# Kernel tuning notes

Hardware: AMD Instinct MI355X
Metric: run time of the kernel (lower is better)

The kernel has to match this reference:

```python
import jax, jax.numpy as jnp
import numpy as np

B, N = 128, 256
EPS = float(np.finfo(np.float32).eps)  # torch clamp_probs epsilon for fp32


def to_z(logits, u):
    # torch.distributions.utils.clamp_probs + Gumbel perturbation
    uc = jnp.clip(u, EPS, 1.0 - EPS)
    return logits + (-jnp.log(-jnp.log(uc)))


def _find_cycle(heads):
    # heads[j] = parent of j; node 0 is the root (heads[0] == 0).
    L = len(heads)
    color = np.zeros(L, dtype=np.int8)  # 0 unvisited, 1 on path, 2 done
    color[0] = 2
    for start in range(1, L):
        if color[start]:
            continue
        path = []
        v = start
        while color[v] == 0:
            color[v] = 1
            path.append(v)
            v = int(heads[v])
        if color[v] == 1:  # found a cycle
            i = path.index(v)
            return path[i:]
        for p in path:
            color[p] = 2
    return None


def _chu_liu(score):
    # score[h, d] = weight of edge h -> d; diag and column 0 are -inf.
    L = score.shape[0]
    heads = score.argmax(axis=0)
    heads[0] = 0
    cyc = _find_cycle(heads)
    if cyc is None:
        return heads
    cyc = np.asarray(cyc)
    mask = np.ones(L, dtype=bool)
    mask[cyc] = False
    non = np.where(mask)[0]  # includes root 0
    n = len(non)
    cyc_head_sc = score[heads[cyc], cyc]  # [|C|] chosen in-edge weights of cycle nodes
    # contracted score matrix: nodes = non-cycle nodes + one supernode (index n)
    new = np.full((n + 1, n + 1), -np.inf, dtype=score.dtype)
    new[:n, :n] = score[np.ix_(non, non)]
    into = score[np.ix_(non, cyc)] - cyc_head_sc[None, :]  # gain of entering cycle at each node
    arg_into = into.argmax(axis=1)
    new[:n, n] = into[np.arange(n), arg_into]
    outo = score[np.ix_(cyc, non)]
    arg_out = outo.argmax(axis=0)
    new[n, :n] = outo[arg_out, np.arange(n)]
    nh = _chu_liu(new)
    # expand
    heads_out = np.empty(L, dtype=np.int64)
    nh_non = nh[:n]
    safe = np.clip(nh_non, 0, n - 1)
    heads_out[non] = np.where(nh_non == n, cyc[arg_out], non[safe])
    heads_out[cyc] = heads[cyc]
    hc = int(nh[n])  # head of the contracted supernode (index into non)
    heads_out[cyc[arg_into[hc]]] = non[hc]  # break the cycle at the entry node
    heads_out[0] = 0
    return heads_out


def edmonds_batch(z, lengths):
    # z: np [B, N, N] edge scores z[b, h, d]; root = node 0; per-graph size lengths[b].
    Bn, Nn, _ = z.shape
    arb = np.zeros((Bn, Nn, Nn), dtype=np.float32)
    stats = np.zeros((Bn,), dtype=np.float32)
    for b in range(Bn):  # irregular sequential graph algorithm: per-graph host loop
        L = int(lengths[b])
        s = z[b, :L, :L].astype(np.float64).copy()
        np.fill_diagonal(s, -np.inf)
        s[:, 0] = -np.inf  # no incoming edges to root
        heads = _chu_liu(s)
        deps = np.arange(1, L)
        arb[b, heads[deps], deps] = 1.0
        stats[b] = z[b, heads[deps], deps].sum()
    return jnp.asarray(arb), jnp.asarray(stats)


def setup_inputs():
    key = jax.random.key(0)
    k1, k2, k3 = jax.random.split(key, 3)
    logits = jax.random.normal(k1, (B, N, N), dtype=jnp.float32)
    u = jax.random.uniform(k2, (B, N, N), dtype=jnp.float32)
    lengths = jax.random.randint(k3, (B,), 2, N + 1, dtype=jnp.int32)
    return {"logits": logits, "u": u, "lengths": lengths}


def reference(logits, u, lengths):
    z = to_z(logits, u)  # Gumbel-perturbed scores (differentiable part)
    arb, stats = edmonds_batch(np.asarray(z), np.asarray(lengths))
    return (arb, stats, z)
```

## Files before the change

### kernel.cpp

```cpp
#include <hip/hip_runtime.h>
#include <cmath>

static constexpr int Bn = 128;
static constexpr int Nn = 256;
static constexpr int META_PB = 131072;

template <typename T>
__global__ __launch_bounds__(256) void zinit_kernel(
    const float* __restrict__ logits,
    const float* __restrict__ u,
    float* __restrict__ zout,
    float* __restrict__ arb,
    T* __restrict__ M)
{
    int idx = blockIdx.x * blockDim.x + threadIdx.x;
    int j = idx & (Nn - 1);
    int i = (idx >> 8) & (Nn - 1);
    const float EPS = 1.1920928955078125e-07f;
    float uv = u[idx];
    uv = fminf(fmaxf(uv, EPS), 1.0f - EPS);
    float z = logits[idx] - logf(-logf(uv));
    zout[idx] = z;
    arb[idx] = 0.0f;
    M[idx] = (i == j || j == 0) ? (T)(-INFINITY) : (T)z;
}

template <typename T>
__global__ __launch_bounds__(256) void edmonds_kernel(
    const int* __restrict__ lengths,
    const float* __restrict__ zout,
    T* __restrict__ Mg,
    unsigned char* __restrict__ metag,
    float* __restrict__ arb,
    float* __restrict__ stats)
{
    const int b = blockIdx.x;
    const int t = threadIdx.x;
    const int lane = t & 63, wv = t >> 6;
    T* M = Mg + (size_t)b * (Nn * Nn);
    unsigned char* meta = metag + (size_t)b * META_PB;
    const float* zb = zout + (size_t)b * (Nn * Nn);

    __shared__ unsigned short act[256];
    __shared__ unsigned short h[256];
    __shared__ unsigned short h2[256];
    __shared__ unsigned short p1[256];
    __shared__ unsigned short p2[256];
    __shared__ unsigned short inv_[256];
    __shared__ unsigned short cyc_c[256];
    __shared__ unsigned short non_c[256];
    __shared__ unsigned short cslot_s[256];
    __shared__ unsigned short resc[256];
    __shared__ unsigned short lev_n[256], lev_c[256];
    __shared__ int lev_off[256];
    __shared__ unsigned char in_cyc[256];
    __shared__ T hval[256];
    __shared__ T chs[256];
    __shared__ double red[256];
    __shared__ unsigned wmin[4];
    __shared__ int wcnt[4];
    __shared__ int sh_clen, sh_cnt, sh_wslot;

    const int L = lengths[b];

    act[t] = (unsigned short)t;
    if (t < L) {
        T best = -INFINITY; int bi = 0;
        const T* col = M + t;
        int i = 0;
        for (; i + 8 <= L; i += 8) {
            T v[8];
            #pragma unroll
            for (int k = 0; k < 8; ++k) v[k] = col[(i + k) * Nn];
            #pragma unroll
            for (int k = 0; k < 8; ++k)
                if (v[k] > best) { best = v[k]; bi = i + k; }
        }
        for (; i < L; ++i) {
            T v = col[i * Nn];
            if (v > best) { best = v; bi = i; }
        }
        h[t] = (t == 0) ? (unsigned short)0 : (unsigned short)bi;
        hval[t] = best;
    }
    __syncthreads();

    int Lc = L, depth = 0, moff = 0;

    while (true) {
        in_cyc[t] = 0;
        if (t < Lc) p1[t] = h[t];
        __syncthreads();

        const int rounds = 32 - __clz(Lc - 1);
        unsigned short* pa = p1;
        unsigned short* pb = p2;
        for (int r = 0; r < rounds; ++r) {
            if (t < Lc) pb[t] = pa[pa[t]];
            __syncthreads();
            unsigned short* tmp = pa; pa = pb; pb = tmp;
        }

        unsigned cand = (t >= 1 && t < Lc && pa[t] != 0) ? (unsigned)t : 0xFFFFu;
        for (int m = 1; m < 64; m <<= 1)
            cand = min(cand, (unsigned)__shfl_xor((int)cand, m));
        if (lane == 0) wmin[wv] = cand;
        __syncthreads();
        const unsigned vstar = min(min(wmin[0], wmin[1]), min(wmin[2], wmin[3]));
        if (vstar == 0xFFFFu) break;

        if (t == 0) {
            int w = pa[vstar];
            int cl = 0, v = w;
            do { cyc_c[cl++] = (unsigned short)v; in_cyc[v] = 1; v = h[v]; }
            while (v != w);
            sh_clen = cl;
            sh_wslot = act[w];
            sh_cnt = 0;
        }
        __syncthreads();
        const int clen = sh_clen;
        const int n = Lc - clen;
        const int wslot = sh_wslot;

        const bool fl = (t < Lc) && !in_cyc[t];
        unsigned long long mask = __ballot(fl);
        if (lane == 0) wcnt[wv] = __popcll(mask);
        __syncthreads();
        if (fl) {
            int base = 0;
            for (int k = 0; k < wv; ++k) base += wcnt[k];
            int pos = base + __popcll(mask & ((1ull << lane) - 1ull));
            non_c[pos] = (unsigned short)t;
            inv_[t] = (unsigned short)pos;
        }
        if (t < clen) {
            const int cc = cyc_c[t];
            chs[t] = hval[cc];
            cslot_s[t] = act[cc];
        }
        __syncthreads();

        T vin_r = (T)0, vout_r = (T)0;
        unsigned char argin_r = 0, argout_r = 0;
        int slot_r = 0;
        if (t < n) {
            slot_r = act[non_c[t]];
            T bv = -INFINITY; int bi = 0;
            T bo = -INFINITY; int bj = 0;
            int c = 0;
            for (; c + 4 <= clen; c += 4) {
                int cs[4]; T ch[4];
                #pragma unroll
                for (int k = 0; k < 4; ++k) { cs[k] = cslot_s[c + k]; ch[k] = chs[c + k]; }
                T vi[4], vo[4];
                #pragma unroll
                for (int k = 0; k < 4; ++k) {
                    vi[k] = M[slot_r * Nn + cs[k]] - ch[k];
                    vo[k] = M[cs[k] * Nn + slot_r];
                }
                #pragma unroll
                for (int k = 0; k < 4; ++k) {
                    if (vi[k] > bv) { bv = vi[k]; bi = c + k; }
                    if (vo[k] > bo) { bo = vo[k]; bj = c + k; }
                }
            }
            for (; c < clen; ++c) {
                const int cs = cslot_s[c];
                T vi = M[slot_r * Nn + cs] - chs[c];
                T vo = M[cs * Nn + slot_r];
                if (vi > bv) { bv = vi; bi = c; }
                if (vo > bo) { bo = vo; bj = c; }
            }
            vin_r = bv; argin_r = (unsigned char)bi;
            vout_r = bo; argout_r = (unsigned char)bj;
        }

        unsigned char* mp = meta + moff;
        if (t < n) {
            mp[t] = (unsigned char)non_c[t];
            mp[n + t] = argin_r;
            mp[2 * n + t] = argout_r;
            M[slot_r * Nn + wslot] = vin_r;
            M[wslot * Nn + slot_r] = vout_r;
        }
        if (t < clen) {
            mp[3 * n + t] = (unsigned char)cyc_c[t];
            mp[3 * n + clen + t] = (unsigned char)h[cyc_c[t]];
        }
        if (t == 0) {
            M[wslot * Nn + wslot] = (T)(-INFINITY);
            lev_n[depth] = (unsigned short)n;
            lev_c[depth] = (unsigned short)clen;
            lev_off[depth] = moff;
        }
        unsigned short myact = 0, myh = 0; T myhval = (T)0; bool need = false;
        if (t < n) {
            const int oc = non_c[t];
            myact = act[oc];
            const int ho = h[oc];
            need = (in_cyc[ho] != 0);
            if (!need) { myh = inv_[ho]; myhval = hval[oc]; }
        }
        __syncthreads();

        if (t < n) {
            act[t] = myact;
            if (!need) { h[t] = myh; hval[t] = myhval; }
            else { int kk = atomicAdd(&sh_cnt, 1); resc[kk] = (unsigned short)t; }
        }
        if (t == 0) {
            act[n] = (unsigned short)wslot;
            int kk = atomicAdd(&sh_cnt, 1); resc[kk] = (unsigned short)n;
        }
        __syncthreads();
        moff += 3 * n + 2 * clen;
        ++depth;
        Lc = n + 1;

        const int nr = sh_cnt;
        if (t < nr) {
            const int jc = resc[t];
            const int cslot = act[jc];
            T best = -INFINITY; int bi = 0;
            int i = 0;
            for (; i + 8 <= Lc; i += 8) {
                int rows[8];
                #pragma unroll
                for (int k = 0; k < 8; ++k) rows[k] = act[i + k];
                T v[8];
                #pragma unroll
                for (int k = 0; k < 8; ++k) v[k] = M[rows[k] * Nn + cslot];
                #pragma unroll
                for (int k = 0; k < 8; ++k)
                    if (v[k] > best) { best = v[k]; bi = i + k; }
            }
            for (; i < Lc; ++i) {
                T v = M[(int)act[i] * Nn + cslot];
                if (v > best) { best = v; bi = i; }
            }
            h[jc] = (unsigned short)bi;
            hval[jc] = best;
        }
        if (t == 0) h[0] = 0;
        __syncthreads();
    }

    unsigned short* hcur = h;
    unsigned short* hnew = h2;
    for (int lvl = depth - 1; lvl >= 0; --lvl) {
        const int n = lev_n[lvl];
        const int c = lev_c[lvl];
        const unsigned char* mp = meta + lev_off[lvl];
        const unsigned char* pnon    = mp;
        const unsigned char* pargin  = mp + n;
        const unsigned char* pargout = mp + 2 * n;
        const unsigned char* pcyc    = mp + 3 * n;
        const unsigned char* phcyc   = mp + 3 * n + c;
        if (t < n) {
            const int x = hcur[t];
            hnew[pnon[t]] = (x == n) ? (unsigned short)pcyc[pargout[t]]
                                     : (unsigned short)pnon[x];
        }
        if (t < c) hnew[pcyc[t]] = phcyc[t];
        __syncthreads();
        if (t == 0) {
            const int hc = hcur[n];
            hnew[pcyc[pargin[hc]]] = pnon[hc];
            hnew[0] = 0;
        }
        __syncthreads();
        unsigned short* tmp = hcur; hcur = hnew; hnew = tmp;
    }

    double acc = 0.0;
    if (t >= 1 && t < L) {
        const int hd = hcur[t];
        arb[(size_t)b * (Nn * Nn) + hd * Nn + t] = 1.0f;
        acc = (double)zb[hd * Nn + t];
    }
    red[t] = acc;
    __syncthreads();
    for (int s = 128; s > 0; s >>= 1) {
        if (t < s) red[t] += red[t + s];
        __syncthreads();
    }
    if (t == 0) stats[b] = (float)red[0];
}

extern "C" void kernel_launch(void* const* d_in, const int* in_sizes, int n_in,
                              void* d_out, int out_size, void* d_ws, size_t ws_size,
                              hipStream_t stream)
{
    const float* logits  = (const float*)d_in[0];
    const float* u       = (const float*)d_in[1];
    const int*   lengths = (const int*)d_in[2];

    float* out   = (float*)d_out;
    float* arb   = out;
    float* stats = out + (size_t)Bn * Nn * Nn;
    float* zout  = stats + Bn;

    const int total = Bn * Nn * Nn;
    const int zblocks = total / 256;

    const size_t needD = (size_t)Bn * Nn * Nn * sizeof(double) + (size_t)Bn * META_PB;

    if (ws_size >= needD) {
        double* M = (double*)d_ws;
        unsigned char* meta = (unsigned char*)d_ws + (size_t)Bn * Nn * Nn * sizeof(double);
        zinit_kernel<double><<<zblocks, 256, 0, stream>>>(logits, u, zout, arb, M);
        edmonds_kernel<double><<<Bn, 256, 0, stream>>>(lengths, zout, M, meta, arb, stats);
    } else {
        float* M = (float*)d_ws;
        unsigned char* meta = (unsigned char*)d_ws + (size_t)Bn * Nn * Nn * sizeof(float);
        zinit_kernel<float><<<zblocks, 256, 0, stream>>>(logits, u, zout, arb, M);
        edmonds_kernel<float><<<Bn, 256, 0, stream>>>(lengths, zout, M, meta, arb, stats);
    }
}
```

Before: 752.8 us.

## Contract all cycles per Chu-Liu/Edmonds level instead of one cycle

The per-graph Edmonds loop now marks every node that lies on a cycle of the current head graph and contracts all cycles into supernodes in a single level, rather than finding and contracting one cycle per iteration. In- and out-edge scores for each supernode are computed with per-cycle argmax loops, and the expansion phase is generalised to break each cycle at its own entry node. The aim is to cut the number of sequential contraction levels, each of which costs pointer-jumping and block barriers. In exchange it adds a serial cycle walk on one thread, extra metadata bytes per level, and per-thread loops over every cycle.

```diff
diff --git a/kernel.cpp b/kernel.cpp
--- a/kernel.cpp
+++ b/kernel.cpp
@@ -38,7 +38,7 @@
     const int t = threadIdx.x;
     const int lane = t & 63, wv = t >> 6;
     T* M = Mg + (size_t)b * (Nn * Nn);
-    unsigned char* meta = metag + (size_t)b * META_PB;
+    unsigned char* mp = metag + (size_t)b * META_PB;
     const float* zb = zout + (size_t)b * (Nn * Nn);
 
     __shared__ unsigned short act[256];
@@ -47,19 +47,22 @@
     __shared__ unsigned short p1[256];
     __shared__ unsigned short p2[256];
     __shared__ unsigned short inv_[256];
-    __shared__ unsigned short cyc_c[256];
+    __shared__ unsigned short cycnodes[256];
+    __shared__ unsigned short cmem[256];
+    __shared__ unsigned short cmemhead[256];
     __shared__ unsigned short non_c[256];
-    __shared__ unsigned short cslot_s[256];
     __shared__ unsigned short resc[256];
-    __shared__ unsigned short lev_n[256], lev_c[256];
+    __shared__ unsigned short coff[130];
+    __shared__ unsigned short wsl[129];
+    __shared__ unsigned short lev_n[256], lev_ncyc[256], lev_Lc[256];
     __shared__ int lev_off[256];
     __shared__ unsigned char in_cyc[256];
+    __shared__ unsigned char cid[256];
     __shared__ T hval[256];
-    __shared__ T chs[256];
+    __shared__ T chsm[256];
     __shared__ double red[256];
-    __shared__ unsigned wmin[4];
-    __shared__ int wcnt[4];
-    __shared__ int sh_clen, sh_cnt, sh_wslot;
+    __shared__ int wcntC[4], wcntS[4];
+    __shared__ int sh_ncyc, sh_cnt;
 
     const int L = lengths[b];
 
@@ -89,6 +92,7 @@
 
     while (true) {
         in_cyc[t] = 0;
+        cid[t] = 0xFF;
         if (t < Lc) p1[t] = h[t];
         __syncthreads();
 
@@ -101,122 +105,136 @@
             unsigned short* tmp = pa; pa = pb; pb = tmp;
         }
 
-        unsigned cand = (t >= 1 && t < Lc && pa[t] != 0) ? (unsigned)t : 0xFFFFu;
-        for (int m = 1; m < 64; m <<= 1)
-            cand = min(cand, (unsigned)__shfl_xor((int)cand, m));
-        if (lane == 0) wmin[wv] = cand;
-        __syncthreads();
-        const unsigned vstar = min(min(wmin[0], wmin[1]), min(wmin[2], wmin[3]));
-        if (vstar == 0xFFFFu) break;
+        if (t < Lc && pa[t] != 0) in_cyc[pa[t]] = 1;
+        __syncthreads();
+
+        const bool isC = (t < Lc) && in_cyc[t];
+        const bool isS = (t < Lc) && !in_cyc[t];
+        unsigned long long mC = __ballot(isC);
+        unsigned long long mS = __ballot(isS);
+        if (lane == 0) { wcntC[wv] = __popcll(mC); wcntS[wv] = __popcll(mS); }
+        __syncthreads();
+        const int ncn = wcntC[0] + wcntC[1] + wcntC[2] + wcntC[3];
+        if (ncn == 0) break;
+        const int n = Lc - ncn;
+        {
+            int baseC = 0, baseS = 0;
+            for (int k = 0; k < wv; ++k) { baseC += wcntC[k]; baseS += wcntS[k]; }
+            if (isC) {
+                int pos = baseC + __popcll(mC & ((1ull << lane) - 1ull));
+                cycnodes[pos] = (unsigned short)t;
+            }
+            if (isS) {
+                int pos = baseS + __popcll(mS & ((1ull << lane) - 1ull));
+                non_c[pos] = (unsigned short)t;
+                inv_[t] = (unsigned short)pos;
+            }
+        }
+        __syncthreads();
 
         if (t == 0) {
-            int w = pa[vstar];
-            int cl = 0, v = w;
-            do { cyc_c[cl++] = (unsigned short)v; in_cyc[v] = 1; v = h[v]; }
-            while (v != w);
-            sh_clen = cl;
-            sh_wslot = act[w];
+            int nc = 0, pos = 0;
+            for (int q = 0; q < ncn; ++q) {
+                const int s = cycnodes[q];
+                if (cid[s] != 0xFF) continue;
+                coff[nc] = (unsigned short)pos;
+                int v = s;
+                do {
+                    cmem[pos] = (unsigned short)v;
+                    cid[v] = (unsigned char)nc;
+                    ++pos;
+                    v = h[v];
+                } while (v != s);
+                wsl[nc] = act[s];
+                ++nc;
+            }
+            coff[nc] = (unsigned short)pos;
+            sh_ncyc = nc;
             sh_cnt = 0;
         }
         __syncthreads();
-        const int clen = sh_clen;
-        const int n = Lc - clen;
-        const int wslot = sh_wslot;
-
-        const bool fl = (t < Lc) && !in_cyc[t];
-        unsigned long long mask = __ballot(fl);
-        if (lane == 0) wcnt[wv] = __popcll(mask);
-        __syncthreads();
-        if (fl) {
-            int base = 0;
-            for (int k = 0; k < wv; ++k) base += wcnt[k];
-            int pos = base + __popcll(mask & ((1ull << lane) - 1ull));
-            non_c[pos] = (unsigned short)t;
-            inv_[t] = (unsigned short)pos;
-        }
-        if (t < clen) {
-            const int cc = cyc_c[t];
-            chs[t] = hval[cc];
-            cslot_s[t] = act[cc];
-        }
-        __syncthreads();
-
-        T vin_r = (T)0, vout_r = (T)0;
-        unsigned char argin_r = 0, argout_r = 0;
-        int slot_r = 0;
-        if (t < n) {
-            slot_r = act[non_c[t]];
-            T bv = -INFINITY; int bi = 0;
-            T bo = -INFINITY; int bj = 0;
-            int c = 0;
-            for (; c + 4 <= clen; c += 4) {
-                int cs[4]; T ch[4];
-                #pragma unroll
-                for (int k = 0; k < 4; ++k) { cs[k] = cslot_s[c + k]; ch[k] = chs[c + k]; }
-                T vi[4], vo[4];
-                #pragma unroll
-                for (int k = 0; k < 4; ++k) {
-                    vi[k] = M[slot_r * Nn + cs[k]] - ch[k];
-                    vo[k] = M[cs[k] * Nn + slot_r];
+        const int ncyc = sh_ncyc;
+        const int totmem = Lc - n;
+        const int n_new = n + ncyc;
+
+        if (t < totmem) {
+            chsm[t] = hval[cmem[t]];
+            cmemhead[t] = h[cmem[t]];
+        }
+        __syncthreads();
+
+        const int o_non  = moff;
+        const int o_mem  = moff + n;
+        const int o_mh   = o_mem + totmem;
+        const int o_aout = o_mh + totmem;
+        const int o_ain  = o_aout + ncyc * Lc;
+        if (t < n) mp[o_non + t] = (unsigned char)non_c[t];
+        if (t < totmem) {
+            mp[o_mem + t] = (unsigned char)cmem[t];
+            mp[o_mh + t] = (unsigned char)cmemhead[t];
+        }
+
+        if (t < Lc) {
+            const int cslot = act[t];
+            for (int k = 0; k < ncyc; ++k) {
+                T bo = -INFINITY; int bp = coff[k];
+                for (int pos = coff[k]; pos < coff[k + 1]; ++pos) {
+                    T v = M[(int)act[cmem[pos]] * Nn + cslot];
+                    if (v > bo) { bo = v; bp = pos; }
                 }
-                #pragma unroll
-                for (int k = 0; k < 4; ++k) {
-                    if (vi[k] > bv) { bv = vi[k]; bi = c + k; }
-                    if (vo[k] > bo) { bo = vo[k]; bj = c + k; }
+                M[(int)wsl[k] * Nn + cslot] = bo;
+                mp[o_aout + k * Lc + t] = (unsigned char)bp;
+            }
+        }
+        __syncthreads();
+
+        if (t < n_new) {
+            const int slot_x = (t < n) ? (int)act[non_c[t]] : (int)wsl[t - n];
+            for (int k = 0; k < ncyc; ++k) {
+                if (t == n + k) {
+                    M[(int)wsl[k] * Nn + (int)wsl[k]] = (T)(-INFINITY);
+                    continue;
                 }
-            }
-            for (; c < clen; ++c) {
-                const int cs = cslot_s[c];
-                T vi = M[slot_r * Nn + cs] - chs[c];
-                T vo = M[cs * Nn + slot_r];
-                if (vi > bv) { bv = vi; bi = c; }
-                if (vo > bo) { bo = vo; bj = c; }
-            }
-            vin_r = bv; argin_r = (unsigned char)bi;
-            vout_r = bo; argout_r = (unsigned char)bj;
-        }
-
-        unsigned char* mp = meta + moff;
-        if (t < n) {
-            mp[t] = (unsigned char)non_c[t];
-            mp[n + t] = argin_r;
-            mp[2 * n + t] = argout_r;
-            M[slot_r * Nn + wslot] = vin_r;
-            M[wslot * Nn + slot_r] = vout_r;
-        }
-        if (t < clen) {
-            mp[3 * n + t] = (unsigned char)cyc_c[t];
-            mp[3 * n + clen + t] = (unsigned char)h[cyc_c[t]];
-        }
-        if (t == 0) {
-            M[wslot * Nn + wslot] = (T)(-INFINITY);
-            lev_n[depth] = (unsigned short)n;
-            lev_c[depth] = (unsigned short)clen;
-            lev_off[depth] = moff;
-        }
-        unsigned short myact = 0, myh = 0; T myhval = (T)0; bool need = false;
+                T bv = -INFINITY; int bp = coff[k];
+                for (int pos = coff[k]; pos < coff[k + 1]; ++pos) {
+                    T v = M[slot_x * Nn + (int)act[cmem[pos]]] - chsm[pos];
+                    if (v > bv) { bv = v; bp = pos; }
+                }
+                M[slot_x * Nn + (int)wsl[k]] = bv;
+                mp[o_ain + k * n_new + t] = (unsigned char)bp;
+            }
+        }
+
+        unsigned short myact = 0, myh = 0; T myhval = (T)0; bool alive = false;
         if (t < n) {
             const int oc = non_c[t];
             myact = act[oc];
             const int ho = h[oc];
-            need = (in_cyc[ho] != 0);
-            if (!need) { myh = inv_[ho]; myhval = hval[oc]; }
+            alive = (cid[ho] == 0xFF);
+            if (alive) { myh = inv_[ho]; myhval = hval[oc]; }
         }
         __syncthreads();
 
         if (t < n) {
             act[t] = myact;
-            if (!need) { h[t] = myh; hval[t] = myhval; }
+            if (alive) { h[t] = myh; hval[t] = myhval; }
             else { int kk = atomicAdd(&sh_cnt, 1); resc[kk] = (unsigned short)t; }
         }
+        if (t < ncyc) {
+            act[n + t] = wsl[t];
+            int kk = atomicAdd(&sh_cnt, 1); resc[kk] = (unsigned short)(n + t);
+        }
         if (t == 0) {
-            act[n] = (unsigned short)wslot;
-            int kk = atomicAdd(&sh_cnt, 1); resc[kk] = (unsigned short)n;
-        }
-        __syncthreads();
-        moff += 3 * n + 2 * clen;
+            h[0] = 0;
+            lev_n[depth] = (unsigned short)n;
+            lev_ncyc[depth] = (unsigned short)ncyc;
+            lev_Lc[depth] = (unsigned short)Lc;
+            lev_off[depth] = moff;
+        }
+        __syncthreads();
+        moff += n + 2 * totmem + ncyc * (Lc + n_new);
         ++depth;
-        Lc = n + 1;
+        Lc = n_new;
 
         const int nr = sh_cnt;
         if (t < nr) {
@@ -242,7 +260,6 @@
             h[jc] = (unsigned short)bi;
             hval[jc] = best;
         }
-        if (t == 0) h[0] = 0;
         __syncthreads();
     }
 
@@ -250,25 +267,37 @@
     unsigned short* hnew = h2;
     for (int lvl = depth - 1; lvl >= 0; --lvl) {
         const int n = lev_n[lvl];
-        const int c = lev_c[lvl];
-        const unsigned char* mp = meta + lev_off[lvl];
-        const unsigned char* pnon    = mp;
-        const unsigned char* pargin  = mp + n;
-        const unsigned char* pargout = mp + 2 * n;
-        const unsigned char* pcyc    = mp + 3 * n;
-        const unsigned char* phcyc   = mp + 3 * n + c;
+        const int ncyc = lev_ncyc[lvl];
+        const int Lco = lev_Lc[lvl];
+        const int off = lev_off[lvl];
+        const int totmem = Lco - n;
+        const int n_new = n + ncyc;
+        const int o_mem  = off + n;
+        const int o_mh   = o_mem + totmem;
+        const int o_aout = o_mh + totmem;
+        const int o_ain  = o_aout + ncyc * Lco;
         if (t < n) {
+            const int j = mp[off + t];
             const int x = hcur[t];
-            hnew[pnon[t]] = (x == n) ? (unsigned short)pcyc[pargout[t]]
-                                     : (unsigned short)pnon[x];
-        }
-        if (t < c) hnew[pcyc[t]] = phcyc[t];
-        __syncthreads();
-        if (t == 0) {
-            const int hc = hcur[n];
-            hnew[pcyc[pargin[hc]]] = pnon[hc];
-            hnew[0] = 0;
-        }
+            hnew[j] = (x < n)
+                ? (unsigned short)mp[off + x]
+                : (unsigned short)mp[o_mem + mp[o_aout + (x - n) * Lco + j]];
+        }
+        if (t < totmem) {
+            const int v = mp[o_mem + t];
+            hnew[v] = (unsigned short)mp[o_mh + t];
+        }
+        __syncthreads();
+        if (t < ncyc) {
+            const int hk = hcur[n + t];
+            const int ain = mp[o_ain + t * n_new + hk];
+            const int vstar = mp[o_mem + ain];
+            const int src = (hk < n)
+                ? (int)mp[off + hk]
+                : (int)mp[o_mem + mp[o_aout + (hk - n) * Lco + vstar]];
+            hnew[vstar] = (unsigned short)src;
+        }
+        if (t == 0) hnew[0] = 0;
         __syncthreads();
         unsigned short* tmp = hcur; hcur = hnew; hnew = tmp;
     }
```

Result: slower. 860.3 us (+14.3%).

## Maintain transposed score matrix for coalesced column argmax in Edmonds kernel

Applied to the files above, without the earlier changes.

The init kernel now also writes a transposed copy of the masked score matrix, using a 32x32 shared-memory tile transpose. The Edmonds kernel reads that copy for column scans (head selection and cycle-entry gains), so accesses that were strided by row become contiguous per thread. Contraction writes now update both matrices to keep them consistent. This doubles workspace use and adds extra writes, and the path is only taken when the workspace is large enough.

```diff
diff --git a/kernel.cpp b/kernel.cpp
--- a/kernel.cpp
+++ b/kernel.cpp
@@ -5,31 +5,55 @@
 static constexpr int Nn = 256;
 static constexpr int META_PB = 131072;
 
-template <typename T>
+template <typename T, bool MT>
 __global__ __launch_bounds__(256) void zinit_kernel(
     const float* __restrict__ logits,
     const float* __restrict__ u,
     float* __restrict__ zout,
     float* __restrict__ arb,
-    T* __restrict__ M)
+    T* __restrict__ M,
+    T* __restrict__ MTg)
 {
-    int idx = blockIdx.x * blockDim.x + threadIdx.x;
-    int j = idx & (Nn - 1);
-    int i = (idx >> 8) & (Nn - 1);
+    const int b    = blockIdx.x >> 6;
+    const int tile = blockIdx.x & 63;
+    const int ti = tile >> 3, tj = tile & 7;
+    const int t = threadIdx.x;
+    const int r8 = t >> 5, c = t & 31;
+
+    __shared__ T zt[32][33];
+
     const float EPS = 1.1920928955078125e-07f;
-    float uv = u[idx];
-    uv = fminf(fmaxf(uv, EPS), 1.0f - EPS);
-    float z = logits[idx] - logf(-logf(uv));
-    zout[idx] = z;
-    arb[idx] = 0.0f;
-    M[idx] = (i == j || j == 0) ? (T)(-INFINITY) : (T)z;
+    #pragma unroll
+    for (int s = 0; s < 4; ++s) {
+        const int row = ti * 32 + s * 8 + r8;
+        const int col = tj * 32 + c;
+        const int idx = b * (Nn * Nn) + row * Nn + col;
+        float uv = u[idx];
+        uv = fminf(fmaxf(uv, EPS), 1.0f - EPS);
+        float z = logits[idx] - logf(-logf(uv));
+        zout[idx] = z;
+        arb[idx] = 0.0f;
+        T mval = (row == col || col == 0) ? (T)(-INFINITY) : (T)z;
+        M[idx] = mval;
+        if (MT) zt[s * 8 + r8][c] = mval;
+    }
+    if (MT) {
+        __syncthreads();
+        #pragma unroll
+        for (int s = 0; s < 4; ++s) {
+            const int trow = tj * 32 + s * 8 + r8;
+            const int tcol = ti * 32 + c;
+            MTg[b * (Nn * Nn) + trow * Nn + tcol] = zt[c][s * 8 + r8];
+        }
+    }
 }
 
-template <typename T>
+template <typename T, bool MT>
 __global__ __launch_bounds__(256) void edmonds_kernel(
     const int* __restrict__ lengths,
     const float* __restrict__ zout,
     T* __restrict__ Mg,
+    T* __restrict__ MTgg,
     unsigned char* __restrict__ metag,
     float* __restrict__ arb,
     float* __restrict__ stats)
@@ -38,6 +62,7 @@
     const int t = threadIdx.x;
     const int lane = t & 63, wv = t >> 6;
     T* M = Mg + (size_t)b * (Nn * Nn);
+    T* MT_ = MT ? (MTgg + (size_t)b * (Nn * Nn)) : nullptr;
     unsigned char* meta = metag + (size_t)b * META_PB;
     const float* zb = zout + (size_t)b * (Nn * Nn);
 
@@ -156,7 +181,8 @@
                 T vi[4], vo[4];
                 #pragma unroll
                 for (int k = 0; k < 4; ++k) {
-                    vi[k] = M[slot_r * Nn + cs[k]] - ch[k];
+                    if (MT) vi[k] = MT_[cs[k] * Nn + slot_r] - ch[k];
+                    else    vi[k] = M[slot_r * Nn + cs[k]] - ch[k];
                     vo[k] = M[cs[k] * Nn + slot_r];
                 }
                 #pragma unroll
@@ -167,7 +193,8 @@
             }
             for (; c < clen; ++c) {
                 const int cs = cslot_s[c];
-                T vi = M[slot_r * Nn + cs] - chs[c];
+                T vi = MT ? (MT_[cs * Nn + slot_r] - chs[c])
+                          : (M[slot_r * Nn + cs] - chs[c]);
                 T vo = M[cs * Nn + slot_r];
                 if (vi > bv) { bv = vi; bi = c; }
                 if (vo > bo) { bo = vo; bj = c; }
@@ -183,6 +210,10 @@
             mp[2 * n + t] = argout_r;
             M[slot_r * Nn + wslot] = vin_r;
             M[wslot * Nn + slot_r] = vout_r;
+            if (MT) {
+                MT_[wslot * Nn + slot_r] = vin_r;
+                MT_[slot_r * Nn + wslot] = vout_r;
+            }
         }
         if (t < clen) {
             mp[3 * n + t] = (unsigned char)cyc_c[t];
@@ -190,6 +221,7 @@
         }
         if (t == 0) {
             M[wslot * Nn + wslot] = (T)(-INFINITY);
+            if (MT) MT_[wslot * Nn + wslot] = (T)(-INFINITY);
             lev_n[depth] = (unsigned short)n;
             lev_c[depth] = (unsigned short)clen;
             lev_off[depth] = moff;
@@ -222,6 +254,7 @@
         if (t < nr) {
             const int jc = resc[t];
             const int cslot = act[jc];
+            const T* base = MT ? (MT_ + cslot * Nn) : nullptr;
             T best = -INFINITY; int bi = 0;
             int i = 0;
             for (; i + 8 <= Lc; i += 8) {
@@ -230,13 +263,14 @@
                 for (int k = 0; k < 8; ++k) rows[k] = act[i + k];
                 T v[8];
                 #pragma unroll
-                for (int k = 0; k < 8; ++k) v[k] = M[rows[k] * Nn + cslot];
+                for (int k = 0; k < 8; ++k)
+                    v[k] = MT ? base[rows[k]] : M[rows[k] * Nn + cslot];
                 #pragma unroll
                 for (int k = 0; k < 8; ++k)
                     if (v[k] > best) { best = v[k]; bi = i + k; }
             }
             for (; i < Lc; ++i) {
-                T v = M[(int)act[i] * Nn + cslot];
+                T v = MT ? base[(int)act[i]] : M[(int)act[i] * Nn + cslot];
                 if (v > best) { best = v; bi = i; }
             }
             h[jc] = (unsigned short)bi;
@@ -301,20 +335,27 @@
     float* stats = out + (size_t)Bn * Nn * Nn;
     float* zout  = stats + Bn;
 
-    const int total = Bn * Nn * Nn;
-    const int zblocks = total / 256;
-
-    const size_t needD = (size_t)Bn * Nn * Nn * sizeof(double) + (size_t)Bn * META_PB;
-
-    if (ws_size >= needD) {
+    const size_t mat = (size_t)Bn * Nn * Nn;
+    const size_t metaB = (size_t)Bn * META_PB;
+
+    const size_t needD_MT = 2 * mat * sizeof(double) + metaB;
+    const size_t needD    = mat * sizeof(double) + metaB;
+
+    if (ws_size >= needD_MT) {
+        double* M  = (double*)d_ws;
+        double* MT = M + mat;
+        unsigned char* meta = (unsigned char*)(MT + mat);
+        zinit_kernel<double, true><<<Bn * 64, 256, 0, stream>>>(logits, u, zout, arb, M, MT);
+        edmonds_kernel<double, true><<<Bn, 256, 0, stream>>>(lengths, zout, M, MT, meta, arb, stats);
+    } else if (ws_size >= needD) {
         double* M = (double*)d_ws;
-        unsigned char* meta = (unsigned char*)d_ws + (size_t)Bn * Nn * Nn * sizeof(double);
-        zinit_kernel<double><<<zblocks, 256, 0, stream>>>(logits, u, zout, arb, M);
-        edmonds_kernel<double><<<Bn, 256, 0, stream>>>(lengths, zout, M, meta, arb, stats);
+        unsigned char* meta = (unsigned char*)(M + mat);
+        zinit_kernel<double, false><<<Bn * 64, 256, 0, stream>>>(logits, u, zout, arb, M, nullptr);
+        edmonds_kernel<double, false><<<Bn, 256, 0, stream>>>(lengths, zout, M, nullptr, meta, arb, stats);
     } else {
         float* M = (float*)d_ws;
-        unsigned char* meta = (unsigned char*)d_ws + (size_t)Bn * Nn * Nn * sizeof(float);
-        zinit_kernel<float><<<zblocks, 256, 0, stream>>>(logits, u, zout, arb, M);
-        edmonds_kernel<float><<<Bn, 256, 0, stream>>>(lengths, zout, M, meta, arb, stats);
+        unsigned char* meta = (unsigned char*)(M + mat);
+        zinit_kernel<float, false><<<Bn * 64, 256, 0, stream>>>(logits, u, zout, arb, M, nullptr);
+        edmonds_kernel<float, false><<<Bn, 256, 0, stream>>>(lengths, zout, M, nullptr, meta, arb, stats);
     }
 }
```

After: 906.2 us. 1.2x slower.

## Compact contracted score matrix into smaller dense buffer as graph shrinks

Applied to the files above, without the earlier changes.

Once the number of active nodes falls below a power-of-two stride, the edmonds kernel gathers the active rows and columns into a ping-pong buffer with that smaller stride and resets the active-slot mapping to the identity. Later argmax scans and cycle in/out scans then touch a compact matrix instead of a strided 256-wide one, which is meant to improve cache locality and cut wasted memory traffic. The cost is an extra workspace allocation, an O(Lc^2) copy with two block barriers at each compaction, and a new kernel variant taken only when the workspace is large enough.

```diff
diff --git a/kernel.cpp b/kernel.cpp
--- a/kernel.cpp
+++ b/kernel.cpp
@@ -4,6 +4,7 @@
 static constexpr int Bn = 128;
 static constexpr int Nn = 256;
 static constexpr int META_PB = 131072;
+static constexpr int MC_PB   = 128 * 128;
 
 template <typename T>
 __global__ __launch_bounds__(256) void zinit_kernel(
@@ -25,11 +26,12 @@
     M[idx] = (i == j || j == 0) ? (T)(-INFINITY) : (T)z;
 }
 
-template <typename T>
+template <typename T, bool CP>
 __global__ __launch_bounds__(256) void edmonds_kernel(
     const int* __restrict__ lengths,
     const float* __restrict__ zout,
     T* __restrict__ Mg,
+    T* __restrict__ Mcg,
     unsigned char* __restrict__ metag,
     float* __restrict__ arb,
     float* __restrict__ stats)
@@ -37,9 +39,13 @@
     const int b = blockIdx.x;
     const int t = threadIdx.x;
     const int lane = t & 63, wv = t >> 6;
-    T* M = Mg + (size_t)b * (Nn * Nn);
+    T* bufA = Mg + (size_t)b * (Nn * Nn);
+    T* bufB = CP ? (Mcg + (size_t)b * MC_PB) : nullptr;
     unsigned char* meta = metag + (size_t)b * META_PB;
     const float* zb = zout + (size_t)b * (Nn * Nn);
+
+    T* Mcur = bufA;
+    int S = Nn;
 
     __shared__ unsigned short act[256];
     __shared__ unsigned short h[256];
@@ -66,7 +72,7 @@
     act[t] = (unsigned short)t;
     if (t < L) {
         T best = -INFINITY; int bi = 0;
-        const T* col = M + t;
+        const T* col = Mcur + t;
         int i = 0;
         for (; i + 8 <= L; i += 8) {
             T v[8];
@@ -156,8 +162,8 @@
                 T vi[4], vo[4];
                 #pragma unroll
                 for (int k = 0; k < 4; ++k) {
-                    vi[k] = M[slot_r * Nn + cs[k]] - ch[k];
-                    vo[k] = M[cs[k] * Nn + slot_r];
+                    vi[k] = Mcur[slot_r * S + cs[k]] - ch[k];
+                    vo[k] = Mcur[cs[k] * S + slot_r];
                 }
                 #pragma unroll
                 for (int k = 0; k < 4; ++k) {
@@ -167,8 +173,8 @@
             }
             for (; c < clen; ++c) {
                 const int cs = cslot_s[c];
-                T vi = M[slot_r * Nn + cs] - chs[c];
-                T vo = M[cs * Nn + slot_r];
+                T vi = Mcur[slot_r * S + cs] - chs[c];
+                T vo = Mcur[cs * S + slot_r];
                 if (vi > bv) { bv = vi; bi = c; }
                 if (vo > bo) { bo = vo; bj = c; }
             }
@@ -181,15 +187,15 @@
             mp[t] = (unsigned char)non_c[t];
             mp[n + t] = argin_r;
             mp[2 * n + t] = argout_r;
-            M[slot_r * Nn + wslot] = vin_r;
-            M[wslot * Nn + slot_r] = vout_r;
+            Mcur[slot_r * S + wslot] = vin_r;
+            Mcur[wslot * S + slot_r] = vout_r;
         }
         if (t < clen) {
             mp[3 * n + t] = (unsigned char)cyc_c[t];
             mp[3 * n + clen + t] = (unsigned char)h[cyc_c[t]];
         }
         if (t == 0) {
-            M[wslot * Nn + wslot] = (T)(-INFINITY);
+            Mcur[wslot * S + wslot] = (T)(-INFINITY);
             lev_n[depth] = (unsigned short)n;
             lev_c[depth] = (unsigned short)clen;
             lev_off[depth] = moff;
@@ -230,13 +236,13 @@
                 for (int k = 0; k < 8; ++k) rows[k] = act[i + k];
                 T v[8];
                 #pragma unroll
-                for (int k = 0; k < 8; ++k) v[k] = M[rows[k] * Nn + cslot];
+                for (int k = 0; k < 8; ++k) v[k] = Mcur[rows[k] * S + cslot];
                 #pragma unroll
                 for (int k = 0; k < 8; ++k)
                     if (v[k] > best) { best = v[k]; bi = i + k; }
             }
             for (; i < Lc; ++i) {
-                T v = M[(int)act[i] * Nn + cslot];
+                T v = Mcur[(int)act[i] * S + cslot];
                 if (v > best) { best = v; bi = i; }
             }
             h[jc] = (unsigned short)bi;
@@ -244,6 +250,23 @@
         }
         if (t == 0) h[0] = 0;
         __syncthreads();
+
+        if (CP) {
+            int Snew = (Lc <= 32) ? 32 : (1 << (32 - __clz(Lc - 1)));
+            if (Snew < S) {
+                T* dst = (Mcur == bufA) ? bufB : bufA;
+                for (int i = wv; i < Lc; i += 4) {
+                    const int srow = (int)act[i] * S;
+                    for (int j = lane; j < Lc; j += 64)
+                        dst[i * Snew + j] = Mcur[srow + (int)act[j]];
+                }
+                __syncthreads();
+                if (t < Lc) act[t] = (unsigned short)t;
+                Mcur = dst;
+                S = Snew;
+                __syncthreads();
+            }
+        }
     }
 
     unsigned short* hcur = h;
@@ -304,17 +327,28 @@
     const int total = Bn * Nn * Nn;
     const int zblocks = total / 256;
 
-    const size_t needD = (size_t)Bn * Nn * Nn * sizeof(double) + (size_t)Bn * META_PB;
-
-    if (ws_size >= needD) {
+    const size_t mat = (size_t)Bn * Nn * Nn;
+    const size_t metaB = (size_t)Bn * META_PB;
+    const size_t mcB = (size_t)Bn * MC_PB * sizeof(double);
+
+    const size_t needCP = mat * sizeof(double) + metaB + mcB;
+    const size_t needD  = mat * sizeof(double) + metaB;
+
+    if (ws_size >= needCP) {
         double* M = (double*)d_ws;
-        unsigned char* meta = (unsigned char*)d_ws + (size_t)Bn * Nn * Nn * sizeof(double);
+        unsigned char* meta = (unsigned char*)(M + mat);
+        double* Mc = (double*)((char*)d_ws + mat * sizeof(double) + metaB);
         zinit_kernel<double><<<zblocks, 256, 0, stream>>>(logits, u, zout, arb, M);
-        edmonds_kernel<double><<<Bn, 256, 0, stream>>>(lengths, zout, M, meta, arb, stats);
+        edmonds_kernel<double, true><<<Bn, 256, 0, stream>>>(lengths, zout, M, Mc, meta, arb, stats);
+    } else if (ws_size >= needD) {
+        double* M = (double*)d_ws;
+        unsigned char* meta = (unsigned char*)(M + mat);
+        zinit_kernel<double><<<zblocks, 256, 0, stream>>>(logits, u, zout, arb, M);
+        edmonds_kernel<double, false><<<Bn, 256, 0, stream>>>(lengths, zout, M, nullptr, meta, arb, stats);
     } else {
         float* M = (float*)d_ws;
-        unsigned char* meta = (unsigned char*)d_ws + (size_t)Bn * Nn * Nn * sizeof(float);
+        unsigned char* meta = (unsigned char*)(M + mat);
         zinit_kernel<float><<<zblocks, 256, 0, stream>>>(logits, u, zout, arb, M);
-        edmonds_kernel<float><<<Bn, 256, 0, stream>>>(lengths, zout, M, meta, arb, stats);
+        edmonds_kernel<float, false><<<Bn, 256, 0, stream>>>(lengths, zout, M, nullptr, meta, arb, stats);
     }
 }
```

Result: slower. 787.0 us (+4.5%).
